# Kernel tuning notes

Measured on AMD Instinct MI355X. Metric: run time of the kernel, lower is better.

Reference implementation:

```python
import jax, jax.numpy as jnp
import numpy as np

HEAD_DIM = 64
NUM_HEAD = 8
NUM_CLUSTERS = 16
B, N, M = 2, 2048, 2048


def setup_inputs() -> dict:
    key = jax.random.key(0)
    ks = jax.random.split(key, 10)
    d = HEAD_DIM
    inp = {
        "Q": jax.random.normal(ks[0], (B, NUM_HEAD, N, d), jnp.float32),
        "K": jax.random.normal(ks[1], (B, NUM_HEAD, M, d), jnp.float32),
        "V": jax.random.normal(ks[2], (B, NUM_HEAD, M, d), jnp.float32),
        "mask": jnp.zeros((B, M), jnp.int32),
        "noise": jax.random.uniform(ks[3], (B, NUM_HEAD, N, M), jnp.float32),
        "emb": jax.random.normal(ks[4], (NUM_HEAD * NUM_CLUSTERS, d), jnp.float32),
        "W1": jax.random.normal(ks[5], (d, d), jnp.float32) * 0.02,
        "b1": jnp.zeros((d,), jnp.float32),
        "W2": jax.random.normal(ks[6], (d, d), jnp.float32) * 0.02,
        "b2": jnp.zeros((d,), jnp.float32),
        "W3": jax.random.normal(ks[7], (d, d), jnp.float32) * 0.02,
        "b3": jnp.zeros((d,), jnp.float32),
    }
    return inp


def _proj(x, W1, b1, W2, b2, W3, b3):
    # torch nn.Linear: y = x @ W.T + b; dropout is identity in eval mode
    x = jax.nn.relu(jnp.einsum("bhnd,ed->bhne", x, W1) + b1)
    x = jax.nn.relu(jnp.einsum("bhnd,ed->bhne", x, W2) + b2)
    return jnp.einsum("bhnd,ed->bhne", x, W3) + b3


def reference(Q, K, V, mask, noise, emb, W1, b1, W2, b2, W3, b3):
    b, h, n, d = Q.shape
    m = V.shape[2]
    k = NUM_CLUSTERS

    clusters = emb.reshape(h, k, d)                                  # [h,k,d]
    dist = jnp.einsum("hkd,hjd->hkj", clusters, clusters)            # [h,k,k]
    # softmax over the flattened k*k matrix per head
    S = jax.nn.softmax(dist.reshape(h, k * k), axis=-1).reshape(h, k, k)

    Qhat = jax.nn.sigmoid(jnp.einsum("bhnd,hkd->bhnk", _proj(Q, W1, b1, W2, b2, W3, b3), clusters))
    Khat = jax.nn.sigmoid(jnp.einsum("bhmd,hkd->bhmk", _proj(K, W1, b1, W2, b2, W3, b3), clusters))

    SK = jnp.einsum("hkj,bhmj->bhkm", S, Khat)                       # [b,h,k,m]
    expA = jnp.einsum("bhnk,bhkm->bhnm", Qhat, SK)                   # Bernoulli probs in [0,1]

    # SampleGraphSparseGraph: Bernoulli sample with straight-through gradient
    sample = (noise < expA).astype(Q.dtype)
    graph = expA + jax.lax.stop_gradient(sample - expA)

    dot = jnp.einsum("bhnd,bhmd->bhnm", Q, K) / jnp.sqrt(jnp.asarray(d, Q.dtype))
    dot = jnp.where(mask[:, None, None, :] == 1, -jnp.inf, dot)
    p = jax.nn.softmax(dot, axis=-1) * graph
    # F.normalize(p=1): x / max(||x||_1, 1e-12); p is non-negative
    attn = p / jnp.maximum(jnp.sum(p, axis=-1, keepdims=True), 1e-12)

    X = jnp.einsum("bhnm,bhmd->bhnd", attn, V)
    sparsity = jnp.sum(graph, axis=(0, -1, -2)) / (b * n * m)        # [h]
    return X, sparsity, graph, attn
```

## Files before the change

### kernel.cpp

```cpp
#include <hip/hip_runtime.h>


typedef float  f32x4 __attribute__((ext_vector_type(4)));
typedef float  f32x8 __attribute__((ext_vector_type(8)));
typedef double f64x2 __attribute__((ext_vector_type(2)));
typedef __bf16 bf16x8 __attribute__((ext_vector_type(8)));

__device__ __forceinline__ unsigned short f2bf(float f) {
  __bf16 b = (__bf16)f;
  return __builtin_bit_cast(unsigned short, b);
}

__global__ __launch_bounds__(256) void kS(const float* __restrict__ emb,
                                          double* __restrict__ wsS,
                                          float* __restrict__ wsSP) {
  __shared__ double c[16][65];
  __shared__ double red[256];
  const int t = threadIdx.x, h = blockIdx.x;
  if (t == 0) wsSP[h] = 0.f;
  for (int i = t; i < 1024; i += 256) c[i >> 6][i & 63] = (double)emb[(size_t)h * 1024 + i];
  __syncthreads();
  const int k = t >> 4, j = t & 15;
  double acc = 0.0;
  for (int d = 0; d < 64; ++d) acc += c[k][d] * c[j][d];
  red[t] = acc; __syncthreads();
  for (int s = 128; s > 0; s >>= 1) { if (t < s) red[t] = fmax(red[t], red[t + s]); __syncthreads(); }
  const double mx = red[0]; __syncthreads();
  const double e = exp(acc - mx);
  red[t] = e; __syncthreads();
  for (int s = 128; s > 0; s >>= 1) { if (t < s) red[t] += red[t + s]; __syncthreads(); }
  wsS[h * 256 + t] = e / red[0];
}

__global__ __launch_bounds__(256) void kMLP(
    const float* __restrict__ Q, const float* __restrict__ K,
    const float* __restrict__ emb,
    const float* __restrict__ W1, const float* __restrict__ b1,
    const float* __restrict__ W2, const float* __restrict__ b2,
    const float* __restrict__ W3, const float* __restrict__ b3,
    const double* __restrict__ wsS,
    double* __restrict__ QHAT, double* __restrict__ SKT) {
  __shared__ double Xt[64][65];
  __shared__ float  Wl[64][65];
  __shared__ float  bsS[64];
  __shared__ float  cl[16][65];
  __shared__ double kh[64][17];
  __shared__ double Sl[256];

  const int t = threadIdx.x;
  const int blk = blockIdx.x;
  const int side = blk >> 9;
  const int idx = blk & 511;
  const int bh = idx >> 5;
  const int h = bh & 7;
  const int chunk = idx & 31;
  const size_t t0 = (size_t)bh * 2048 + (size_t)chunk * 64;

  const float* src = side ? K : Q;
  for (int i = t; i < 4096; i += 256) Xt[i >> 6][i & 63] = (double)src[t0 * 64 + i];

  const float* Ws[3] = {W1, W2, W3};
  const float* bs[3] = {b1, b2, b3};
  const int te = t & 15, tt = t >> 4;
  const int e0 = te * 4, tok0 = tt * 4;

  for (int l = 0; l < 3; ++l) {
    __syncthreads();
    for (int i = t; i < 4096; i += 256) Wl[i >> 6][i & 63] = Ws[l][i];
    if (t < 64) bsS[t] = bs[l][t];
    __syncthreads();
    double o[4][4];
#pragma unroll
    for (int i = 0; i < 4; ++i)
#pragma unroll
      for (int j = 0; j < 4; ++j) o[i][j] = 0.0;
    for (int d = 0; d < 64; ++d) {
      const double x0 = Xt[tok0 + 0][d], x1 = Xt[tok0 + 1][d], x2 = Xt[tok0 + 2][d], x3 = Xt[tok0 + 3][d];
      const double w0 = (double)Wl[e0 + 0][d], w1 = (double)Wl[e0 + 1][d];
      const double w2 = (double)Wl[e0 + 2][d], w3 = (double)Wl[e0 + 3][d];
      o[0][0] += x0 * w0; o[0][1] += x0 * w1; o[0][2] += x0 * w2; o[0][3] += x0 * w3;
      o[1][0] += x1 * w0; o[1][1] += x1 * w1; o[1][2] += x1 * w2; o[1][3] += x1 * w3;
      o[2][0] += x2 * w0; o[2][1] += x2 * w1; o[2][2] += x2 * w2; o[2][3] += x2 * w3;
      o[3][0] += x3 * w0; o[3][1] += x3 * w1; o[3][2] += x3 * w2; o[3][3] += x3 * w3;
    }
#pragma unroll
    for (int i = 0; i < 4; ++i)
#pragma unroll
      for (int j = 0; j < 4; ++j) {
        double v = o[i][j] + (double)bsS[e0 + j];
        if (l < 2) v = fmax(v, 0.0);
        o[i][j] = v;
      }
    __syncthreads();
#pragma unroll
    for (int i = 0; i < 4; ++i)
#pragma unroll
      for (int j = 0; j < 4; ++j) Xt[tok0 + i][e0 + j] = o[i][j];
  }
  __syncthreads();
  for (int i = t; i < 1024; i += 256) cl[i >> 6][i & 63] = emb[(size_t)h * 1024 + i];
  if (side) { for (int i = t; i < 256; i += 256) Sl[i] = wsS[h * 256 + i]; }
  __syncthreads();

  const int tok = t >> 2, k0 = (t & 3) * 4;
  double z[4] = {0.0, 0.0, 0.0, 0.0};
  for (int d = 0; d < 64; ++d) {
    const double xv = Xt[tok][d];
    z[0] += xv * (double)cl[k0 + 0][d]; z[1] += xv * (double)cl[k0 + 1][d];
    z[2] += xv * (double)cl[k0 + 2][d]; z[3] += xv * (double)cl[k0 + 3][d];
  }
  double hat[4];
#pragma unroll
  for (int j = 0; j < 4; ++j) hat[j] = 1.0 / (1.0 + exp(-z[j]));

  if (!side) {
#pragma unroll
    for (int j = 0; j < 4; ++j) QHAT[(t0 + tok) * 16 + k0 + j] = hat[j];
  } else {
    kh[tok][k0 + 0] = hat[0]; kh[tok][k0 + 1] = hat[1];
    kh[tok][k0 + 2] = hat[2]; kh[tok][k0 + 3] = hat[3];
    __syncthreads();
    double sk[4] = {0.0, 0.0, 0.0, 0.0};
    for (int jj = 0; jj < 16; ++jj) {
      const double kv = kh[tok][jj];
      sk[0] += Sl[(k0 + 0) * 16 + jj] * kv; sk[1] += Sl[(k0 + 1) * 16 + jj] * kv;
      sk[2] += Sl[(k0 + 2) * 16 + jj] * kv; sk[3] += Sl[(k0 + 3) * 16 + jj] * kv;
    }
#pragma unroll
    for (int j = 0; j < 4; ++j) SKT[(t0 + tok) * 16 + k0 + j] = sk[j];
  }
}

__global__ __launch_bounds__(256, 4) void kSample(
    const float* __restrict__ noise,
    const double* __restrict__ qhat, const double* __restrict__ skt,
    float* __restrict__ wsSP,
    unsigned long long* __restrict__ GB64, float* __restrict__ GOUT) {
  const int t = threadIdx.x;
  const int lane = t & 63, wave = t >> 6;
  const int bh = blockIdx.y, h = bh & 7;
  const int n0 = blockIdx.x * 32;

  int cnt = 0;
  for (int chunk = 0; chunk < 8; ++chunk) {
    const int m = chunk * 256 + wave * 64 + lane;
    double skv[16];
    const double* sp = skt + ((size_t)bh * 2048 + m) * 16;
#pragma unroll
    for (int q = 0; q < 8; ++q) *(f64x2*)(skv + 2 * q) = *(const f64x2*)(sp + 2 * q);
    const float* nzp = noise + ((size_t)bh * 2048 + n0) * 2048 + m;
    unsigned long long* gbp = GB64 + ((size_t)bh * 2048 + n0) * 32 + chunk * 4 + wave;
    float* gop = GOUT + ((size_t)bh * 2048 + n0) * 2048 + m;
    const double* qbase = qhat + ((size_t)bh * 2048 + n0) * 16;

    for (int n = 0; n < 32; n += 2) {
      const float nz0 = nzp[(size_t)n * 2048];
      const float nz1 = nzp[(size_t)(n + 1) * 2048];
      const double* q0 = qbase + (size_t)n * 16;
      const double* q1 = qbase + (size_t)(n + 1) * 16;
      double ea0 = 0.0, ea1 = 0.0;
#pragma unroll
      for (int k = 0; k < 16; ++k) {
        ea0 += q0[k] * skv[k];
        ea1 += q1[k] * skv[k];
      }
      const int g0 = ((double)nz0 < ea0) ? 1 : 0;
      const int g1 = ((double)nz1 < ea1) ? 1 : 0;
      cnt += g0 + g1;
      const unsigned long long b0 = __ballot(g0);
      const unsigned long long b1 = __ballot(g1);
      if (lane == 0) {
        gbp[(size_t)n * 32] = b0;
        gbp[(size_t)(n + 1) * 32] = b1;
      }
      gop[(size_t)n * 2048] = g0 ? 1.0f : 0.0f;
      gop[(size_t)(n + 1) * 2048] = g1 ? 1.0f : 0.0f;
    }
  }
  cnt += __shfl_xor(cnt, 1); cnt += __shfl_xor(cnt, 2); cnt += __shfl_xor(cnt, 4);
  cnt += __shfl_xor(cnt, 8); cnt += __shfl_xor(cnt, 16); cnt += __shfl_xor(cnt, 32);
  if (lane == 0) atomicAdd(&wsSP[h], (float)cnt);
}

__global__ __launch_bounds__(256) void kCvt(const float* __restrict__ K,
                                            const float* __restrict__ V,
                                            unsigned short* __restrict__ KB,
                                            unsigned short* __restrict__ VT) {
  __shared__ float vt[128][65];
  const int t = threadIdx.x;
  const int bh = blockIdx.x, ch = blockIdx.y;
  const size_t base = ((size_t)bh * 2048 + ch * 128) * 64;
  for (int i = t; i < 8192; i += 256) {
    KB[base + i] = f2bf(K[base + i]);
    vt[i >> 6][i & 63] = V[base + i];
  }
  __syncthreads();
  const size_t vbase = (size_t)bh * 64 * 2048 + ch * 128;
  for (int i = t; i < 8192; i += 256) {
    const int d = i >> 7, mm = i & 127;
    VT[vbase + (size_t)d * 2048 + mm] = f2bf(vt[mm][d]);
  }
}

__global__ __launch_bounds__(256, 4) void kAttn(
    const float* __restrict__ Q, const int* __restrict__ maskp,
    const unsigned short* __restrict__ KB, const unsigned short* __restrict__ VT,
    const unsigned int* __restrict__ GB32,
    float* __restrict__ XOUT, float* __restrict__ AOUT) {
  __shared__ unsigned int bitsS[16][64];
  __shared__ unsigned short stageS[4][16][32];
  __shared__ float dredS[4][16];
  __shared__ float dinvS[16];
  __shared__ float xredS[16][68];

  const int t = threadIdx.x;
  const int wave = t >> 6, lane = t & 63;
  const int bh = blockIdx.y, b = bh >> 3;
  const int n0 = blockIdx.x * 16;
  const int hi2 = lane >> 4;
  const int hi8 = hi2 << 3;
  const int g4 = hi2 << 2;
  const int lm = lane & 15;

  for (int i = t; i < 1024; i += 256)
    bitsS[i >> 6][i & 63] = GB32[((size_t)bh * 2048 + n0 + (i >> 6)) * 64 + (i & 63)];
  for (int i = t; i < 16 * 68; i += 256) ((float*)xredS)[i] = 0.f;

  const float* qrow = Q + ((size_t)bh * 2048 + n0 + lm) * 64;
  bf16x8 aq[2];
#pragma unroll
  for (int hh = 0; hh < 2; ++hh) {
    const int d0 = hi8 + hh * 32;
    const f32x4 qa = *(const f32x4*)(qrow + d0);
    const f32x4 qb = *(const f32x4*)(qrow + d0 + 4);
    bf16x8 v;
    v[0] = (__bf16)qa[0]; v[1] = (__bf16)qa[1]; v[2] = (__bf16)qa[2]; v[3] = (__bf16)qa[3];
    v[4] = (__bf16)qb[0]; v[5] = (__bf16)qb[1]; v[6] = (__bf16)qb[2]; v[7] = (__bf16)qb[3];
    aq[hh] = v;
  }

  const unsigned short* kbp = KB + (size_t)bh * 2048 * 64;
  const unsigned short* vtp = VT + (size_t)bh * 64 * 2048;
  const int* mkp = maskp + b * 2048;
  __syncthreads();

  float dsum[4] = {0.f, 0.f, 0.f, 0.f};
  for (int it = 0; it < 16; ++it) {
    const int mb = ((it << 2) + wave) << 5;
    f32x4 st[2];
#pragma unroll
    for (int tt = 0; tt < 2; ++tt) {
      const unsigned short* kr = kbp + (size_t)(mb + tt * 16 + lm) * 64 + hi8;
      const bf16x8 b0 = *(const bf16x8*)(kr);
      const bf16x8 b1 = *(const bf16x8*)(kr + 32);
      f32x4 acc = (f32x4){0.f, 0.f, 0.f, 0.f};
      acc = __builtin_amdgcn_mfma_f32_16x16x32_bf16(aq[0], b0, acc, 0, 0, 0);
      acc = __builtin_amdgcn_mfma_f32_16x16x32_bf16(aq[1], b1, acc, 0, 0, 0);
      st[tt] = acc;
    }
#pragma unroll
    for (int tt = 0; tt < 2; ++tt) {
      const int mv = mkp[mb + tt * 16 + lm];
      const f32x4 sv4 = st[tt];
#pragma unroll
      for (int r = 0; r < 4; ++r) {
        const int g = (bitsS[g4 + r][mb >> 5] >> (tt * 16 + lm)) & 1;
        if (g && !mv) dsum[r] += __expf(sv4[r] * 0.125f);
      }
    }
  }
#pragma unroll
  for (int r = 0; r < 4; ++r) {
    float v = dsum[r];
    v += __shfl_xor(v, 1); v += __shfl_xor(v, 2); v += __shfl_xor(v, 4); v += __shfl_xor(v, 8);
    if (lm == 0) dredS[wave][g4 + r] = v;
  }
  __syncthreads();
  if (t < 16) {
    const float dv = dredS[0][t] + dredS[1][t] + dredS[2][t] + dredS[3][t];
    dinvS[t] = 1.0f / fmaxf(dv, 1e-12f);
  }
  __syncthreads();

  const size_t rowbase = (size_t)bh * 2048 + n0;
  f32x4 xacc[4];
#pragma unroll
  for (int td = 0; td < 4; ++td) xacc[td] = (f32x4){0.f, 0.f, 0.f, 0.f};

  for (int it = 0; it < 16; ++it) {
    const int mb = ((it << 2) + wave) << 5;
    f32x4 st[2];
#pragma unroll
    for (int tt = 0; tt < 2; ++tt) {
      const unsigned short* kr = kbp + (size_t)(mb + tt * 16 + lm) * 64 + hi8;
      const bf16x8 b0 = *(const bf16x8*)(kr);
      const bf16x8 b1 = *(const bf16x8*)(kr + 32);
      f32x4 acc = (f32x4){0.f, 0.f, 0.f, 0.f};
      acc = __builtin_amdgcn_mfma_f32_16x16x32_bf16(aq[0], b0, acc, 0, 0, 0);
      acc = __builtin_amdgcn_mfma_f32_16x16x32_bf16(aq[1], b1, acc, 0, 0, 0);
      st[tt] = acc;
    }
#pragma unroll
    for (int tt = 0; tt < 2; ++tt) {
      const int mv = mkp[mb + tt * 16 + lm];
      const f32x4 sv4 = st[tt];
#pragma unroll
      for (int r = 0; r < 4; ++r) {
        const int row = g4 + r;
        const int g = (bitsS[row][mb >> 5] >> (tt * 16 + lm)) & 1;
        const float u = (g && !mv) ? __expf(sv4[r] * 0.125f) : 0.f;
        const int col = tt * 16 + lm;
        stageS[wave][row][col ^ (((row >> 2) & 3) << 3)] = f2bf(u);
      }
    }
    {
      const int rdcol = hi8 ^ (((lm >> 2) & 3) << 3);
      const bf16x8 ua = *(const bf16x8*)&stageS[wave][lm][rdcol];
#pragma unroll
      for (int td = 0; td < 4; ++td) {
        const bf16x8 vb = *(const bf16x8*)(vtp + (size_t)(td * 16 + lm) * 2048 + mb + hi8);
        xacc[td] = __builtin_amdgcn_mfma_f32_16x16x32_bf16(ua, vb, xacc[td], 0, 0, 0);
      }
    }
    {
      const int row = lane >> 2, q = lane & 3;
      const int rc = (q * 8) ^ (((row >> 2) & 3) << 3);
      const unsigned short* up = &stageS[wave][row][rc];
      const float inv = dinvS[row];
      f32x8 av;
#pragma unroll
      for (int j = 0; j < 8; ++j) av[j] = (float)__builtin_bit_cast(__bf16, up[j]) * inv;
      *(f32x8*)(AOUT + (rowbase + row) * 2048 + mb + q * 8) = av;
    }
  }

  for (int w = 0; w < 4; ++w) {
    if (wave == w) {
#pragma unroll
      for (int td = 0; td < 4; ++td)
#pragma unroll
        for (int r = 0; r < 4; ++r) xredS[g4 + r][td * 16 + lm] += xacc[td][r];
    }
    __syncthreads();
  }
  for (int i = t; i < 1024; i += 256) {
    const int nl = i >> 6, d = i & 63;
    XOUT[(rowbase + nl) * 64 + d] = xredS[nl][d] * dinvS[nl];
  }
}

__global__ void kFin(const float* __restrict__ wsSP, float* __restrict__ SPOUT) {
  const int t = threadIdx.x;
  if (t < 8) SPOUT[t] = wsSP[t] * (1.0f / 8388608.0f);
}

extern "C" void kernel_launch(void* const* d_in, const int* in_sizes, int n_in,
                              void* d_out, int out_size, void* d_ws, size_t ws_size,
                              hipStream_t stream) {
  const float* Q = (const float*)d_in[0];
  const float* K = (const float*)d_in[1];
  const float* V = (const float*)d_in[2];
  const int* mask = (const int*)d_in[3];
  const float* noise = (const float*)d_in[4];
  const float* emb = (const float*)d_in[5];
  const float* W1 = (const float*)d_in[6];
  const float* b1 = (const float*)d_in[7];
  const float* W2 = (const float*)d_in[8];
  const float* b2 = (const float*)d_in[9];
  const float* W3 = (const float*)d_in[10];
  const float* b3 = (const float*)d_in[11];

  char* ws = (char*)d_ws;
  double* wsS = (double*)(ws + 0);
  float* wsSP = (float*)(ws + 16384);
  double* QHAT = (double*)(ws + 32768);
  double* SKT  = (double*)(ws + 32768 + 4194304);
  unsigned short* KB = (unsigned short*)(ws + 32768);
  unsigned short* VT = (unsigned short*)(ws + 32768 + 4194304);
  unsigned long long* GB64 = (unsigned long long*)(ws + 32768 + 8388608);
  unsigned int* GB32 = (unsigned int*)(ws + 32768 + 8388608);

  float* out = (float*)d_out;
  float* XOUT = out;
  float* SPOUT = out + 2097152;
  float* GOUT = out + 2097160;
  float* AOUT = out + 69206024;

  kS<<<8, 256, 0, stream>>>(emb, wsS, wsSP);
  kMLP<<<1024, 256, 0, stream>>>(Q, K, emb, W1, b1, W2, b2, W3, b3, wsS, QHAT, SKT);
  kSample<<<dim3(64, 16), 256, 0, stream>>>(noise, QHAT, SKT, wsSP, GB64, GOUT);
  kCvt<<<dim3(16, 16), 256, 0, stream>>>(K, V, KB, VT);
  kAttn<<<dim3(128, 16), 256, 0, stream>>>(Q, mask, KB, VT, GB32, XOUT, AOUT);
  kFin<<<1, 64, 0, stream>>>(wsSP, SPOUT);
}
```

Before: 522.5 us.

## Retile sampling kernel over 2D n/m grid and reorder attention key partition

The sampling kernel now uses a 3D grid where each block covers 64 query rows and a 512-column slab of keys. Each thread keeps two SK vectors resident in registers for the whole block instead of reloading them per chunk, and each Qhat row load is shared across two columns. The occupancy hint on launch bounds is dropped. In the attention kernel, each wave now walks a contiguous 512-key range instead of interleaved 32-key tiles, which changes the memory access locality of K/VT reads and the per-row bitmask accesses.

```diff
diff --git a/kernel.cpp b/kernel.cpp
--- a/kernel.cpp
+++ b/kernel.cpp
@@ -131,51 +131,60 @@
   }
 }
 
-__global__ __launch_bounds__(256, 4) void kSample(
+__global__ __launch_bounds__(256) void kSample(
     const float* __restrict__ noise,
     const double* __restrict__ qhat, const double* __restrict__ skt,
     float* __restrict__ wsSP,
     unsigned long long* __restrict__ GB64, float* __restrict__ GOUT) {
   const int t = threadIdx.x;
   const int lane = t & 63, wave = t >> 6;
-  const int bh = blockIdx.y, h = bh & 7;
-  const int n0 = blockIdx.x * 32;
+  const int nt = blockIdx.x;
+  const int mt = blockIdx.y;
+  const int bh = blockIdx.z, h = bh & 7;
+  const int n0 = nt * 64;
+  const int mA = mt * 512 + wave * 64 + lane;
+  const int mB = mA + 256;
+
+  double skvA[16], skvB[16];
+  {
+    const double* spA = skt + ((size_t)bh * 2048 + mA) * 16;
+    const double* spB = skt + ((size_t)bh * 2048 + mB) * 16;
+#pragma unroll
+    for (int q = 0; q < 8; ++q) {
+      *(f64x2*)(skvA + 2 * q) = *(const f64x2*)(spA + 2 * q);
+      *(f64x2*)(skvB + 2 * q) = *(const f64x2*)(spB + 2 * q);
+    }
+  }
+
+  const double* qbase = qhat + ((size_t)bh * 2048 + n0) * 16;
+  const float* nzbase = noise + ((size_t)bh * 2048 + n0) * 2048;
+  float* gobase = GOUT + ((size_t)bh * 2048 + n0) * 2048;
+  unsigned long long* gbbase = GB64 + ((size_t)bh * 2048 + n0) * 32;
+  const int gA = mA >> 6, gB = mB >> 6;
 
   int cnt = 0;
-  for (int chunk = 0; chunk < 8; ++chunk) {
-    const int m = chunk * 256 + wave * 64 + lane;
-    double skv[16];
-    const double* sp = skt + ((size_t)bh * 2048 + m) * 16;
-#pragma unroll
-    for (int q = 0; q < 8; ++q) *(f64x2*)(skv + 2 * q) = *(const f64x2*)(sp + 2 * q);
-    const float* nzp = noise + ((size_t)bh * 2048 + n0) * 2048 + m;
-    unsigned long long* gbp = GB64 + ((size_t)bh * 2048 + n0) * 32 + chunk * 4 + wave;
-    float* gop = GOUT + ((size_t)bh * 2048 + n0) * 2048 + m;
-    const double* qbase = qhat + ((size_t)bh * 2048 + n0) * 16;
-
-    for (int n = 0; n < 32; n += 2) {
-      const float nz0 = nzp[(size_t)n * 2048];
-      const float nz1 = nzp[(size_t)(n + 1) * 2048];
-      const double* q0 = qbase + (size_t)n * 16;
-      const double* q1 = qbase + (size_t)(n + 1) * 16;
-      double ea0 = 0.0, ea1 = 0.0;
-#pragma unroll
-      for (int k = 0; k < 16; ++k) {
-        ea0 += q0[k] * skv[k];
-        ea1 += q1[k] * skv[k];
-      }
-      const int g0 = ((double)nz0 < ea0) ? 1 : 0;
-      const int g1 = ((double)nz1 < ea1) ? 1 : 0;
-      cnt += g0 + g1;
-      const unsigned long long b0 = __ballot(g0);
-      const unsigned long long b1 = __ballot(g1);
-      if (lane == 0) {
-        gbp[(size_t)n * 32] = b0;
-        gbp[(size_t)(n + 1) * 32] = b1;
-      }
-      gop[(size_t)n * 2048] = g0 ? 1.0f : 0.0f;
-      gop[(size_t)(n + 1) * 2048] = g1 ? 1.0f : 0.0f;
-    }
+  for (int n = 0; n < 64; ++n) {
+    const double* qr = qbase + (size_t)n * 16;
+    double ea0 = 0.0, ea1 = 0.0;
+#pragma unroll
+    for (int k = 0; k < 16; ++k) {
+      const double qk = qr[k];
+      ea0 += qk * skvA[k];
+      ea1 += qk * skvB[k];
+    }
+    const float nzA = nzbase[(size_t)n * 2048 + mA];
+    const float nzB = nzbase[(size_t)n * 2048 + mB];
+    const int g0 = ((double)nzA < ea0) ? 1 : 0;
+    const int g1 = ((double)nzB < ea1) ? 1 : 0;
+    cnt += g0 + g1;
+    const unsigned long long b0 = __ballot(g0);
+    const unsigned long long b1 = __ballot(g1);
+    if (lane == 0) {
+      gbbase[(size_t)n * 32 + gA] = b0;
+      gbbase[(size_t)n * 32 + gB] = b1;
+    }
+    gobase[(size_t)n * 2048 + mA] = g0 ? 1.0f : 0.0f;
+    gobase[(size_t)n * 2048 + mB] = g1 ? 1.0f : 0.0f;
   }
   cnt += __shfl_xor(cnt, 1); cnt += __shfl_xor(cnt, 2); cnt += __shfl_xor(cnt, 4);
   cnt += __shfl_xor(cnt, 8); cnt += __shfl_xor(cnt, 16); cnt += __shfl_xor(cnt, 32);
@@ -246,7 +255,7 @@
 
   float dsum[4] = {0.f, 0.f, 0.f, 0.f};
   for (int it = 0; it < 16; ++it) {
-    const int mb = ((it << 2) + wave) << 5;
+    const int mb = (wave << 9) + (it << 5);
     f32x4 st[2];
 #pragma unroll
     for (int tt = 0; tt < 2; ++tt) {
@@ -288,7 +297,7 @@
   for (int td = 0; td < 4; ++td) xacc[td] = (f32x4){0.f, 0.f, 0.f, 0.f};
 
   for (int it = 0; it < 16; ++it) {
-    const int mb = ((it << 2) + wave) << 5;
+    const int mb = (wave << 9) + (it << 5);
     f32x4 st[2];
 #pragma unroll
     for (int tt = 0; tt < 2; ++tt) {
@@ -388,7 +397,7 @@
 
   kS<<<8, 256, 0, stream>>>(emb, wsS, wsSP);
   kMLP<<<1024, 256, 0, stream>>>(Q, K, emb, W1, b1, W2, b2, W3, b3, wsS, QHAT, SKT);
-  kSample<<<dim3(64, 16), 256, 0, stream>>>(noise, QHAT, SKT, wsSP, GB64, GOUT);
+  kSample<<<dim3(32, 4, 16), 256, 0, stream>>>(noise, QHAT, SKT, wsSP, GB64, GOUT);
   kCvt<<<dim3(16, 16), 256, 0, stream>>>(K, V, KB, VT);
   kAttn<<<dim3(128, 16), 256, 0, stream>>>(Q, mask, KB, VT, GB32, XOUT, AOUT);
   kFin<<<1, 64, 0, stream>>>(wsSP, SPOUT);
```

After: 512.1 us. -2.0%, faster.
